# Performance work log

Measured on AMD Instinct MI355X. Metric: run time of the kernel, lower is better.

The kernel has to match this reference:

```python
import jax, jax.numpy as jnp
import numpy as np

N_NODES = 50000
N_EDGES = 800000
N_EVAL = 500000
D = 96


def _sage_conv(x, edge_index, W_l, W_r, b):
    # PyG SAGEConv with aggr='add':
    #   aggr_out[v] = sum_{(u->v) in edges} x[u]
    #   out = aggr_out @ W_l^T-equivalent + b + x @ W_r  (we store W as [in, out])
    src, dst = edge_index[0], edge_index[1]
    msgs = x[src]                                        # [E, d_in] irregular gather
    aggr = jax.ops.segment_sum(msgs, dst, num_segments=x.shape[0])  # [N, d_in]
    return aggr @ W_l + b + x @ W_r                      # [N, d_out]


def setup_inputs() -> dict:
    key = jax.random.key(0)
    ks = jax.random.split(key, 8)
    scale = 1.0 / np.sqrt(D)
    Features = jax.random.normal(ks[0], (N_NODES, D), dtype=jnp.float32)
    A = jax.random.randint(ks[1], (2, N_EDGES), 0, N_NODES, dtype=jnp.int64)
    E = jax.random.randint(ks[2], (2, N_EVAL), 0, N_NODES, dtype=jnp.int64)
    W1_l = jax.random.normal(ks[3], (D, D), dtype=jnp.float32) * scale
    W1_r = jax.random.normal(ks[4], (D, D), dtype=jnp.float32) * scale
    b1 = jnp.zeros((D,), dtype=jnp.float32)
    W2_l = jax.random.normal(ks[5], (D, D), dtype=jnp.float32) * scale
    W2_r = jax.random.normal(ks[6], (D, D), dtype=jnp.float32) * scale
    b2 = jnp.zeros((D,), dtype=jnp.float32)
    return {"Features": Features, "A": A, "E": E,
            "W1_l": W1_l, "W1_r": W1_r, "b1": b1,
            "W2_l": W2_l, "W2_r": W2_r, "b2": b2}


def reference(Features, A, E, W1_l, W1_r, b1, W2_l, W2_r, b2):
    h = _sage_conv(Features, A, W1_l, W1_r, b1)          # [N, hidden]
    h = jax.nn.relu(h)
    # dropout in eval mode = identity
    h = _sage_conv(h, A, W2_l, W2_r, b2)                 # [N, out]
    # edge scoring: gather src/dst embeddings, dot, sigmoid
    src = h[E[0]]                                        # [n_eval, out]
    dst = h[E[1]]                                        # [n_eval, out]
    return jax.nn.sigmoid(jnp.sum(src * dst, axis=-1))   # [n_eval]
```

## Files before the change

kernel.cpp:

```cpp
#include <hip/hip_runtime.h>
#include <math.h>

#define N_NODES 50000
#define N_EDGES 800000
#define N_EVAL  500000
#define CSTRIDE 16
#define MAXDEG  64
#define NB_GEMM ((N_NODES + 63) / 64)
#define NB_AGG  ((N_NODES * 24 + 255) / 256)
#define HALF_EVAL (N_EVAL / 2)

__device__ __forceinline__ float4 f4add(float4 a, float4 b) {
    return make_float4(a.x + b.x, a.y + b.y, a.z + b.z, a.w + b.w);
}
__device__ __forceinline__ float4 f4fma(float s, float4 w, float4 a) {
    return make_float4(fmaf(s, w.x, a.x), fmaf(s, w.y, a.y),
                       fmaf(s, w.z, a.z), fmaf(s, w.w, a.w));
}
__device__ __forceinline__ float4 ld4(const float* p) {
    return *(const float4*)p;
}


__device__ __forceinline__ void bucket_role(int idx, const int* __restrict__ src,
                                            const int* __restrict__ dst,
                                            int* __restrict__ degS,
                                            unsigned short* __restrict__ bucket) {
    int t = idx * 256 + threadIdx.x;
    if (t < N_EDGES / 4) {
        int4 s = ((const int4*)src)[t];
        int4 d = ((const int4*)dst)[t];
        int r0 = atomicAdd(&degS[(size_t)d.x * CSTRIDE], 1);
        int r1 = atomicAdd(&degS[(size_t)d.y * CSTRIDE], 1);
        int r2 = atomicAdd(&degS[(size_t)d.z * CSTRIDE], 1);
        int r3 = atomicAdd(&degS[(size_t)d.w * CSTRIDE], 1);
        if (r0 < MAXDEG) bucket[(size_t)d.x * MAXDEG + r0] = (unsigned short)s.x;
        if (r1 < MAXDEG) bucket[(size_t)d.y * MAXDEG + r1] = (unsigned short)s.y;
        if (r2 < MAXDEG) bucket[(size_t)d.z * MAXDEG + r2] = (unsigned short)s.z;
        if (r3 < MAXDEG) bucket[(size_t)d.w * MAXDEG + r3] = (unsigned short)s.w;
    }
}

__device__ __forceinline__ float4 aggr_compute16(int v, int c,
        const float* __restrict__ x, const int* __restrict__ degC,
        const unsigned short* __restrict__ bucket) {
    const float* xp = x + c * 4;
    const int4* bk4 = (const int4*)(bucket + (size_t)v * MAXDEG);
    int deg = degC[v];
    int4 p0 = bk4[0], p1 = bk4[1], p2 = bk4[2], p3 = bk4[3];
    int idx[32];
    idx[0]  = p0.x & 0xffff; idx[1]  = (int)((unsigned)p0.x >> 16);
    idx[2]  = p0.y & 0xffff; idx[3]  = (int)((unsigned)p0.y >> 16);
    idx[4]  = p0.z & 0xffff; idx[5]  = (int)((unsigned)p0.z >> 16);
    idx[6]  = p0.w & 0xffff; idx[7]  = (int)((unsigned)p0.w >> 16);
    idx[8]  = p1.x & 0xffff; idx[9]  = (int)((unsigned)p1.x >> 16);
    idx[10] = p1.y & 0xffff; idx[11] = (int)((unsigned)p1.y >> 16);
    idx[12] = p1.z & 0xffff; idx[13] = (int)((unsigned)p1.z >> 16);
    idx[14] = p1.w & 0xffff; idx[15] = (int)((unsigned)p1.w >> 16);
    idx[16] = p2.x & 0xffff; idx[17] = (int)((unsigned)p2.x >> 16);
    idx[18] = p2.y & 0xffff; idx[19] = (int)((unsigned)p2.y >> 16);
    idx[20] = p2.z & 0xffff; idx[21] = (int)((unsigned)p2.z >> 16);
    idx[22] = p2.w & 0xffff; idx[23] = (int)((unsigned)p2.w >> 16);
    idx[24] = p3.x & 0xffff; idx[25] = (int)((unsigned)p3.x >> 16);
    idx[26] = p3.y & 0xffff; idx[27] = (int)((unsigned)p3.y >> 16);
    idx[28] = p3.z & 0xffff; idx[29] = (int)((unsigned)p3.z >> 16);
    idx[30] = p3.w & 0xffff; idx[31] = (int)((unsigned)p3.w >> 16);

    const float4 z = make_float4(0.f, 0.f, 0.f, 0.f);
    float4 t0, t1, t2, t3, t4, t5, t6, t7, t8, t9, t10, t11, t12, t13, t14, t15;
    if (deg >= 16) {
        t0  = ld4(xp + (size_t)idx[0]  * 96);
        t1  = ld4(xp + (size_t)idx[1]  * 96);
        t2  = ld4(xp + (size_t)idx[2]  * 96);
        t3  = ld4(xp + (size_t)idx[3]  * 96);
        t4  = ld4(xp + (size_t)idx[4]  * 96);
        t5  = ld4(xp + (size_t)idx[5]  * 96);
        t6  = ld4(xp + (size_t)idx[6]  * 96);
        t7  = ld4(xp + (size_t)idx[7]  * 96);
        t8  = ld4(xp + (size_t)idx[8]  * 96);
        t9  = ld4(xp + (size_t)idx[9]  * 96);
        t10 = ld4(xp + (size_t)idx[10] * 96);
        t11 = ld4(xp + (size_t)idx[11] * 96);
        t12 = ld4(xp + (size_t)idx[12] * 96);
        t13 = ld4(xp + (size_t)idx[13] * 96);
        t14 = ld4(xp + (size_t)idx[14] * 96);
        t15 = ld4(xp + (size_t)idx[15] * 96);
    } else if (deg >= 8) {
        t0 = ld4(xp + (size_t)idx[0] * 96);
        t1 = ld4(xp + (size_t)idx[1] * 96);
        t2 = ld4(xp + (size_t)idx[2] * 96);
        t3 = ld4(xp + (size_t)idx[3] * 96);
        t4 = ld4(xp + (size_t)idx[4] * 96);
        t5 = ld4(xp + (size_t)idx[5] * 96);
        t6 = ld4(xp + (size_t)idx[6] * 96);
        t7 = ld4(xp + (size_t)idx[7] * 96);
        t8 = z; t9 = z; t10 = z; t11 = z; t12 = z; t13 = z; t14 = z; t15 = z;
        if (deg > 8)  t8  = ld4(xp + (size_t)idx[8]  * 96);
        if (deg > 9)  t9  = ld4(xp + (size_t)idx[9]  * 96);
        if (deg > 10) t10 = ld4(xp + (size_t)idx[10] * 96);
        if (deg > 11) t11 = ld4(xp + (size_t)idx[11] * 96);
        if (deg > 12) t12 = ld4(xp + (size_t)idx[12] * 96);
        if (deg > 13) t13 = ld4(xp + (size_t)idx[13] * 96);
        if (deg > 14) t14 = ld4(xp + (size_t)idx[14] * 96);
    } else {
        t0 = z; t1 = z; t2 = z; t3 = z; t4 = z; t5 = z; t6 = z; t7 = z;
        t8 = z; t9 = z; t10 = z; t11 = z; t12 = z; t13 = z; t14 = z; t15 = z;
        if (deg > 0) t0 = ld4(xp + (size_t)idx[0] * 96);
        if (deg > 1) t1 = ld4(xp + (size_t)idx[1] * 96);
        if (deg > 2) t2 = ld4(xp + (size_t)idx[2] * 96);
        if (deg > 3) t3 = ld4(xp + (size_t)idx[3] * 96);
        if (deg > 4) t4 = ld4(xp + (size_t)idx[4] * 96);
        if (deg > 5) t5 = ld4(xp + (size_t)idx[5] * 96);
        if (deg > 6) t6 = ld4(xp + (size_t)idx[6] * 96);
    }
    float4 a0 = f4add(f4add(f4add(t0, t1), f4add(t2, t3)),
                      f4add(f4add(t4, t5), f4add(t6, t7)));
    float4 a1 = f4add(f4add(f4add(t8, t9), f4add(t10, t11)),
                      f4add(f4add(t12, t13), f4add(t14, t15)));
    if (deg > 16) {
        float4 u0, u1, u2, u3, u4, u5, u6, u7;
        u0 = ld4(xp + (size_t)idx[16] * 96);
        u1 = z; u2 = z; u3 = z; u4 = z; u5 = z; u6 = z; u7 = z;
        if (deg > 17) u1 = ld4(xp + (size_t)idx[17] * 96);
        if (deg > 18) u2 = ld4(xp + (size_t)idx[18] * 96);
        if (deg > 19) u3 = ld4(xp + (size_t)idx[19] * 96);
        if (deg > 20) u4 = ld4(xp + (size_t)idx[20] * 96);
        if (deg > 21) u5 = ld4(xp + (size_t)idx[21] * 96);
        if (deg > 22) u6 = ld4(xp + (size_t)idx[22] * 96);
        if (deg > 23) u7 = ld4(xp + (size_t)idx[23] * 96);
        a0 = f4add(a0, f4add(f4add(u0, u1), f4add(u2, u3)));
        a1 = f4add(a1, f4add(f4add(u4, u5), f4add(u6, u7)));
    }
    if (deg > 24) {
        float4 u0, u1, u2, u3, u4, u5, u6, u7;
        u0 = ld4(xp + (size_t)idx[24] * 96);
        u1 = z; u2 = z; u3 = z; u4 = z; u5 = z; u6 = z; u7 = z;
        if (deg > 25) u1 = ld4(xp + (size_t)idx[25] * 96);
        if (deg > 26) u2 = ld4(xp + (size_t)idx[26] * 96);
        if (deg > 27) u3 = ld4(xp + (size_t)idx[27] * 96);
        if (deg > 28) u4 = ld4(xp + (size_t)idx[28] * 96);
        if (deg > 29) u5 = ld4(xp + (size_t)idx[29] * 96);
        if (deg > 30) u6 = ld4(xp + (size_t)idx[30] * 96);
        if (deg > 31) u7 = ld4(xp + (size_t)idx[31] * 96);
        a0 = f4add(a0, f4add(f4add(u0, u1), f4add(u2, u3)));
        a1 = f4add(a1, f4add(f4add(u4, u5), f4add(u6, u7)));
    }
    if (deg > 32) {
        const unsigned short* bk = bucket + (size_t)v * MAXDEG;
        for (int i = 32; i < deg; ++i)
            a0 = f4add(a0, ld4(xp + (size_t)bk[i] * 96));
    }
    return f4add(a0, a1);
}

__device__ __forceinline__ void aggr_role(int idx, const float* __restrict__ x,
                                          const int* __restrict__ degC,
                                          const unsigned short* __restrict__ bucket,
                                          float* __restrict__ out) {
    int gt = idx * 256 + threadIdx.x;
    if (gt >= N_NODES * 24) return;
    int v = gt / 24;
    int c = gt - v * 24;
    float4 res = aggr_compute16(v, c, x, degC, bucket);
    *(float4*)(out + (size_t)v * 96 + c * 4) = res;
}

__device__ __forceinline__ void selfgemm_role(int g, const float* __restrict__ X,
                                              const float* __restrict__ W96,
                                              const float* __restrict__ bias,
                                              float* __restrict__ S,
                                              float* __restrict__ Ws,
                                              float* __restrict__ xT) {
    const int tid = threadIdx.x;
    const int j   = tid & 31;
    const int ty  = tid >> 5;
    const int v0  = g * 64;

    float acc[8][3];
    float b0 = bias[j], b1 = bias[j + 32], b2 = bias[j + 64];
    #pragma unroll
    for (int r = 0; r < 8; ++r) { acc[r][0] = b0; acc[r][1] = b1; acc[r][2] = b2; }

    const int sr = tid >> 2;
    const int sc = tid & 3;
    int sv = v0 + sr; if (sv >= N_NODES) sv = N_NODES - 1;

    for (int kc = 0; kc < 3; ++kc) {
        const float* W = W96 + kc * (32 * 96);
        const int kbase = kc * 32;
        __syncthreads();
        #pragma unroll
        for (int i = 0; i < 3; ++i) {
            int f = tid + i * 256;
            *(float4*)(Ws + f * 4) = *(const float4*)(W + f * 4);
        }
        {
            const float* rowp = X + (size_t)sv * 96 + kbase;
            float4 a = *(const float4*)(rowp + sc * 4);
            float4 b = *(const float4*)(rowp + sc * 4 + 16);
            int k0 = sc * 4;
            xT[(k0 + 0) * 68 + sr] = a.x;
            xT[(k0 + 1) * 68 + sr] = a.y;
            xT[(k0 + 2) * 68 + sr] = a.z;
            xT[(k0 + 3) * 68 + sr] = a.w;
            xT[(k0 + 16) * 68 + sr] = b.x;
            xT[(k0 + 17) * 68 + sr] = b.y;
            xT[(k0 + 18) * 68 + sr] = b.z;
            xT[(k0 + 19) * 68 + sr] = b.w;
        }
        __syncthreads();
        #pragma unroll 8
        for (int kk = 0; kk < 32; ++kk) {
            float w0 = Ws[kk * 96 + j];
            float w1 = Ws[kk * 96 + j + 32];
            float w2 = Ws[kk * 96 + j + 64];
            float4 xa = *(const float4*)(xT + kk * 68 + ty * 8);
            float4 xb = *(const float4*)(xT + kk * 68 + ty * 8 + 4);
#define ROWFMA(r, xv)                                   \
            acc[r][0] = fmaf(xv, w0, acc[r][0]);        \
            acc[r][1] = fmaf(xv, w1, acc[r][1]);        \
            acc[r][2] = fmaf(xv, w2, acc[r][2]);
            ROWFMA(0, xa.x) ROWFMA(1, xa.y) ROWFMA(2, xa.z) ROWFMA(3, xa.w)
            ROWFMA(4, xb.x) ROWFMA(5, xb.y) ROWFMA(6, xb.z) ROWFMA(7, xb.w)
#undef ROWFMA
        }
    }
    #pragma unroll
    for (int r = 0; r < 8; ++r) {
        int v = v0 + ty * 8 + r;
        if (v < N_NODES) {
            S[(size_t)v * 96 + j]      = acc[r][0];
            S[(size_t)v * 96 + j + 32] = acc[r][1];
            S[(size_t)v * 96 + j + 64] = acc[r][2];
        }
    }
}


__global__ __launch_bounds__(256) void k_fusedA(const int* __restrict__ src,
                                                const int* __restrict__ dst,
                                                int* __restrict__ degS,
                                                unsigned short* __restrict__ bucket,
                                                const float* __restrict__ X,
                                                const float* __restrict__ Wr,
                                                const float* __restrict__ bias,
                                                float* __restrict__ S) {
    __shared__ float Ws[32 * 96];
    __shared__ float xT[32 * 68];
    int b = blockIdx.x;
    if (b & 1) selfgemm_role(b >> 1, X, Wr, bias, S, Ws, xT);
    else       bucket_role(b >> 1, src, dst, degS, bucket);
}

__global__ __launch_bounds__(256) void k_compact(const int* __restrict__ degS,
                                                 int* __restrict__ degC) {
    int v = blockIdx.x * 256 + threadIdx.x;
    if (v < N_NODES) {
        int d = degS[(size_t)v * CSTRIDE];
        degC[v] = d > MAXDEG ? MAXDEG : d;
    }
}

__global__ __launch_bounds__(256, 4) void k_aggr(const float* __restrict__ x,
                                                 const int* __restrict__ degC,
                                                 const unsigned short* __restrict__ bucket,
                                                 float* __restrict__ out) {
    aggr_role(blockIdx.x, x, degC, bucket, out);
}

__global__ __launch_bounds__(256, 4) void k_fusedC(const float* __restrict__ h1,
                                                   const int* __restrict__ degC,
                                                   const unsigned short* __restrict__ bucket,
                                                   float* __restrict__ aggrOut,
                                                   const float* __restrict__ Wr,
                                                   const float* __restrict__ bias,
                                                   float* __restrict__ S) {
    __shared__ float Ws[32 * 96];
    __shared__ float xT[32 * 68];
    int b = blockIdx.x;
    int g = b / 7, r = b % 7;
    if (r == 3) {
        if (g < NB_GEMM) selfgemm_role(g, h1, Wr, bias, S, Ws, xT);
    } else {
        int idx = g * 6 + (r < 3 ? r : r - 1);
        if (idx < NB_AGG) aggr_role(idx, h1, degC, bucket, aggrOut);
    }
}

template <int RELU>
__global__ __launch_bounds__(192) void k_gemmH(const float* __restrict__ P,
                                               const float* __restrict__ Wl,
                                               const float* __restrict__ S,
                                               float* __restrict__ out) {
    __shared__ float Ws[32 * 96];
    __shared__ float xT[32 * 68];
    const int tid = threadIdx.x;
    const int q   = tid % 24;
    const int rg  = tid / 24;
    const int v0  = blockIdx.x * 64;

    const int  row0 = tid >> 3,         qd0 = tid & 7;
    const int  row1 = (tid + 192) >> 3, qd1 = (tid + 192) & 7;
    const int  row2 = (tid + 384) >> 3, qd2 = (tid + 384) & 7;
    const bool has2 = (tid < 128);
    int sv0 = v0 + row0; if (sv0 >= N_NODES) sv0 = N_NODES - 1;
    int sv1 = v0 + row1; if (sv1 >= N_NODES) sv1 = N_NODES - 1;
    int sv2 = v0 + row2; if (sv2 >= N_NODES) sv2 = N_NODES - 1;

    float4 acc[8];
    #pragma unroll
    for (int r = 0; r < 8; ++r) acc[r] = make_float4(0.f, 0.f, 0.f, 0.f);

    float4 wreg0, wreg1, wreg2, wreg3;
    float4 xreg0, xreg1, xreg2;

    auto load_chunk = [&](int kc) {
        const float* W = Wl + kc * (32 * 96);
        const int kbase = kc * 32;
        wreg0 = *(const float4*)(W + (tid + 0 * 192) * 4);
        wreg1 = *(const float4*)(W + (tid + 1 * 192) * 4);
        wreg2 = *(const float4*)(W + (tid + 2 * 192) * 4);
        wreg3 = *(const float4*)(W + (tid + 3 * 192) * 4);
        xreg0 = *(const float4*)(P + (size_t)sv0 * 96 + kbase + qd0 * 4);
        xreg1 = *(const float4*)(P + (size_t)sv1 * 96 + kbase + qd1 * 4);
        if (has2) xreg2 = *(const float4*)(P + (size_t)sv2 * 96 + kbase + qd2 * 4);
    };
    auto store_chunk = [&]() {
        *(float4*)(Ws + (tid + 0 * 192) * 4) = wreg0;
        *(float4*)(Ws + (tid + 1 * 192) * 4) = wreg1;
        *(float4*)(Ws + (tid + 2 * 192) * 4) = wreg2;
        *(float4*)(Ws + (tid + 3 * 192) * 4) = wreg3;
        int k0 = qd0 * 4;
        xT[(k0 + 0) * 68 + row0] = xreg0.x;
        xT[(k0 + 1) * 68 + row0] = xreg0.y;
        xT[(k0 + 2) * 68 + row0] = xreg0.z;
        xT[(k0 + 3) * 68 + row0] = xreg0.w;
        int k1 = qd1 * 4;
        xT[(k1 + 0) * 68 + row1] = xreg1.x;
        xT[(k1 + 1) * 68 + row1] = xreg1.y;
        xT[(k1 + 2) * 68 + row1] = xreg1.z;
        xT[(k1 + 3) * 68 + row1] = xreg1.w;
        if (has2) {
            int k2 = qd2 * 4;
            xT[(k2 + 0) * 68 + row2] = xreg2.x;
            xT[(k2 + 1) * 68 + row2] = xreg2.y;
            xT[(k2 + 2) * 68 + row2] = xreg2.z;
            xT[(k2 + 3) * 68 + row2] = xreg2.w;
        }
    };

    load_chunk(0);
    for (int kc = 0; kc < 3; ++kc) {
        __syncthreads();
        store_chunk();
        if (kc < 2) load_chunk(kc + 1);
        __syncthreads();
        #pragma unroll 8
        for (int kk = 0; kk < 32; ++kk) {
            float4 w  = *(const float4*)(Ws + kk * 96 + q * 4);
            float4 xa = *(const float4*)(xT + kk * 68 + rg * 8);
            float4 xb = *(const float4*)(xT + kk * 68 + rg * 8 + 4);
            acc[0] = f4fma(xa.x, w, acc[0]);
            acc[1] = f4fma(xa.y, w, acc[1]);
            acc[2] = f4fma(xa.z, w, acc[2]);
            acc[3] = f4fma(xa.w, w, acc[3]);
            acc[4] = f4fma(xb.x, w, acc[4]);
            acc[5] = f4fma(xb.y, w, acc[5]);
            acc[6] = f4fma(xb.z, w, acc[6]);
            acc[7] = f4fma(xb.w, w, acc[7]);
        }
    }
    #pragma unroll
    for (int r = 0; r < 8; ++r) {
        int v = v0 + rg * 8 + r;
        if (v < N_NODES) {
            float4 s4 = *(const float4*)(S + (size_t)v * 96 + q * 4);
            float4 o = f4add(acc[r], s4);
            if (RELU) {
                o.x = fmaxf(o.x, 0.f); o.y = fmaxf(o.y, 0.f);
                o.z = fmaxf(o.z, 0.f); o.w = fmaxf(o.w, 0.f);
            }
            *(float4*)(out + (size_t)v * 96 + q * 4) = o;
        }
    }
}

__global__ __launch_bounds__(256) void k_score(const float* __restrict__ h,
                                               const int* __restrict__ E,
                                               float* __restrict__ out) {
    int t = blockIdx.x * 256 + threadIdx.x;
    int e = t >> 3, sub = t & 7;
    if (e >= HALF_EVAL) return;
    int e2 = e + HALF_EVAL;
    int s0 = E[e];
    int d0 = E[N_EVAL + e];
    int s1 = E[e2];
    int d1 = E[N_EVAL + e2];
    const float* ps0 = h + (size_t)s0 * 96 + sub * 12;
    const float* pd0 = h + (size_t)d0 * 96 + sub * 12;
    const float* ps1 = h + (size_t)s1 * 96 + sub * 12;
    const float* pd1 = h + (size_t)d1 * 96 + sub * 12;
    float4 a0 = ld4(ps0 + 0), a1 = ld4(ps0 + 4), a2 = ld4(ps0 + 8);
    float4 b0 = ld4(pd0 + 0), b1 = ld4(pd0 + 4), b2 = ld4(pd0 + 8);
    float4 c0 = ld4(ps1 + 0), c1 = ld4(ps1 + 4), c2 = ld4(ps1 + 8);
    float4 g0 = ld4(pd1 + 0), g1 = ld4(pd1 + 4), g2 = ld4(pd1 + 8);
    float dot0 = a0.x * b0.x + a0.y * b0.y + a0.z * b0.z + a0.w * b0.w
               + a1.x * b1.x + a1.y * b1.y + a1.z * b1.z + a1.w * b1.w
               + a2.x * b2.x + a2.y * b2.y + a2.z * b2.z + a2.w * b2.w;
    float dot1 = c0.x * g0.x + c0.y * g0.y + c0.z * g0.z + c0.w * g0.w
               + c1.x * g1.x + c1.y * g1.y + c1.z * g1.z + c1.w * g1.w
               + c2.x * g2.x + c2.y * g2.y + c2.z * g2.z + c2.w * g2.w;
    dot0 += __shfl_xor(dot0, 1, 64);
    dot1 += __shfl_xor(dot1, 1, 64);
    dot0 += __shfl_xor(dot0, 2, 64);
    dot1 += __shfl_xor(dot1, 2, 64);
    dot0 += __shfl_xor(dot0, 4, 64);
    dot1 += __shfl_xor(dot1, 4, 64);
    if (sub == 0) {
        out[e]  = 1.f / (1.f + expf(-dot0));
        out[e2] = 1.f / (1.f + expf(-dot1));
    }
}


extern "C" void kernel_launch(void* const* d_in, const int* in_sizes, int n_in,
                              void* d_out, int out_size, void* d_ws, size_t ws_size,
                              hipStream_t stream) {
    const float* Features = (const float*)d_in[0];
    const int*   A        = (const int*)d_in[1];
    const int*   E        = (const int*)d_in[2];
    const float* W1l = (const float*)d_in[3];
    const float* W1r = (const float*)d_in[4];
    const float* b1  = (const float*)d_in[5];
    const float* W2l = (const float*)d_in[6];
    const float* W2r = (const float*)d_in[7];
    const float* b2  = (const float*)d_in[8];
    float* out = (float*)d_out;

    char* p = (char*)d_ws;
    auto alloc = [&](size_t bytes) -> char* {
        char* q = p;
        p += (bytes + 255) & ~(size_t)255;
        return q;
    };
    int*   degS   = (int*)alloc((size_t)N_NODES * CSTRIDE * 4);
    int*   degC   = (int*)alloc((size_t)N_NODES * 4);
    unsigned short* bucket =
        (unsigned short*)alloc((size_t)N_NODES * MAXDEG * 2);
    float* bufA   = (float*)alloc((size_t)N_NODES * 96 * 4);
    float* bufB   = (float*)alloc((size_t)N_NODES * 96 * 4);
    float* bufS   = (float*)alloc((size_t)N_NODES * 96 * 4);

    const int* Asrc = A;
    const int* Adst = A + N_EDGES;

    hipMemsetAsync(degS, 0, (size_t)N_NODES * CSTRIDE * 4, stream);

    k_fusedA<<<2 * NB_GEMM, 256, 0, stream>>>(Asrc, Adst, degS, bucket,
                                              Features, W1r, b1, bufS);
    k_compact<<<(N_NODES + 255) / 256, 256, 0, stream>>>(degS, degC);
    k_aggr<<<NB_AGG, 256, 0, stream>>>(Features, degC, bucket, bufA);
    k_gemmH<1><<<NB_GEMM, 192, 0, stream>>>(bufA, W1l, bufS, bufB);
    k_fusedC<<<7 * NB_GEMM, 256, 0, stream>>>(bufB, degC, bucket, bufA,
                                              W2r, b2, bufS);
    k_gemmH<0><<<NB_GEMM, 192, 0, stream>>>(bufA, W2l, bufS, bufA);
    k_score<<<(HALF_EVAL * 8 + 255) / 256, 256, 0, stream>>>(bufA, E, out);
}
```

Before: 300.2 us.

## Drop compaction kernel, shrink GEMM k-chunks, raise occupancy, use nontemporal stores

Removes the k_compact launch and makes the aggregation read the strided degree array directly, clamping the degree inline. The self-GEMM now uses 16-wide k chunks, which halves its shared-memory footprint, and launch bounds rise to 8 blocks per SM for the fused and aggregation kernels. Output stores switch to nontemporal stores. The risks are higher register pressure under the tighter launch bounds, more syncs per GEMM, strided degree reads that are less coalesced, and nontemporal stores evicting data that later kernels reread.

```diff
diff --git a/kernel.cpp b/kernel.cpp
--- a/kernel.cpp
+++ b/kernel.cpp
@@ -19,6 +19,12 @@
 }
 __device__ __forceinline__ float4 ld4(const float* p) {
     return *(const float4*)p;
+}
+typedef float fnt4 __attribute__((ext_vector_type(4)));
+__device__ __forceinline__ void st4nt(float* p, float4 v) {
+    fnt4 t;
+    t.x = v.x; t.y = v.y; t.z = v.z; t.w = v.w;
+    __builtin_nontemporal_store(t, (fnt4*)p);
 }
 
 
@@ -42,12 +48,13 @@
 }
 
 __device__ __forceinline__ float4 aggr_compute16(int v, int c,
-        const float* __restrict__ x, const int* __restrict__ degC,
+        const float* __restrict__ x, const int* __restrict__ degS,
         const unsigned short* __restrict__ bucket) {
     const float* xp = x + c * 4;
     const int4* bk4 = (const int4*)(bucket + (size_t)v * MAXDEG);
-    int deg = degC[v];
+    int deg = degS[(size_t)v * CSTRIDE];
     int4 p0 = bk4[0], p1 = bk4[1], p2 = bk4[2], p3 = bk4[3];
+    if (deg > MAXDEG) deg = MAXDEG;
     int idx[32];
     idx[0]  = p0.x & 0xffff; idx[1]  = (int)((unsigned)p0.x >> 16);
     idx[2]  = p0.y & 0xffff; idx[3]  = (int)((unsigned)p0.y >> 16);
@@ -154,15 +161,15 @@
 }
 
 __device__ __forceinline__ void aggr_role(int idx, const float* __restrict__ x,
-                                          const int* __restrict__ degC,
+                                          const int* __restrict__ degS,
                                           const unsigned short* __restrict__ bucket,
                                           float* __restrict__ out) {
     int gt = idx * 256 + threadIdx.x;
     if (gt >= N_NODES * 24) return;
     int v = gt / 24;
     int c = gt - v * 24;
-    float4 res = aggr_compute16(v, c, x, degC, bucket);
-    *(float4*)(out + (size_t)v * 96 + c * 4) = res;
+    float4 res = aggr_compute16(v, c, x, degS, bucket);
+    st4nt(out + (size_t)v * 96 + c * 4, res);
 }
 
 __device__ __forceinline__ void selfgemm_role(int g, const float* __restrict__ X,
@@ -185,32 +192,24 @@
     const int sc = tid & 3;
     int sv = v0 + sr; if (sv >= N_NODES) sv = N_NODES - 1;
 
-    for (int kc = 0; kc < 3; ++kc) {
-        const float* W = W96 + kc * (32 * 96);
-        const int kbase = kc * 32;
+    for (int kc = 0; kc < 6; ++kc) {
+        const float* W = W96 + kc * (16 * 96);
+        const int kbase = kc * 16;
         __syncthreads();
-        #pragma unroll
-        for (int i = 0; i < 3; ++i) {
-            int f = tid + i * 256;
-            *(float4*)(Ws + f * 4) = *(const float4*)(W + f * 4);
-        }
+        *(float4*)(Ws + tid * 4) = ld4(W + tid * 4);
+        if (tid < 128)
+            *(float4*)(Ws + (tid + 256) * 4) = ld4(W + (tid + 256) * 4);
         {
-            const float* rowp = X + (size_t)sv * 96 + kbase;
-            float4 a = *(const float4*)(rowp + sc * 4);
-            float4 b = *(const float4*)(rowp + sc * 4 + 16);
+            float4 a = ld4(X + (size_t)sv * 96 + kbase + sc * 4);
             int k0 = sc * 4;
             xT[(k0 + 0) * 68 + sr] = a.x;
             xT[(k0 + 1) * 68 + sr] = a.y;
             xT[(k0 + 2) * 68 + sr] = a.z;
             xT[(k0 + 3) * 68 + sr] = a.w;
-            xT[(k0 + 16) * 68 + sr] = b.x;
-            xT[(k0 + 17) * 68 + sr] = b.y;
-            xT[(k0 + 18) * 68 + sr] = b.z;
-            xT[(k0 + 19) * 68 + sr] = b.w;
         }
         __syncthreads();
         #pragma unroll 8
-        for (int kk = 0; kk < 32; ++kk) {
+        for (int kk = 0; kk < 16; ++kk) {
             float w0 = Ws[kk * 96 + j];
             float w1 = Ws[kk * 96 + j + 32];
             float w2 = Ws[kk * 96 + j + 64];
@@ -229,61 +228,52 @@
     for (int r = 0; r < 8; ++r) {
         int v = v0 + ty * 8 + r;
         if (v < N_NODES) {
-            S[(size_t)v * 96 + j]      = acc[r][0];
-            S[(size_t)v * 96 + j + 32] = acc[r][1];
-            S[(size_t)v * 96 + j + 64] = acc[r][2];
-        }
-    }
-}
-
-
-__global__ __launch_bounds__(256) void k_fusedA(const int* __restrict__ src,
-                                                const int* __restrict__ dst,
-                                                int* __restrict__ degS,
-                                                unsigned short* __restrict__ bucket,
-                                                const float* __restrict__ X,
-                                                const float* __restrict__ Wr,
-                                                const float* __restrict__ bias,
-                                                float* __restrict__ S) {
-    __shared__ float Ws[32 * 96];
-    __shared__ float xT[32 * 68];
+            __builtin_nontemporal_store(acc[r][0], &S[(size_t)v * 96 + j]);
+            __builtin_nontemporal_store(acc[r][1], &S[(size_t)v * 96 + j + 32]);
+            __builtin_nontemporal_store(acc[r][2], &S[(size_t)v * 96 + j + 64]);
+        }
+    }
+}
+
+
+__global__ __launch_bounds__(256, 8) void k_fusedA(const int* __restrict__ src,
+                                                   const int* __restrict__ dst,
+                                                   int* __restrict__ degS,
+                                                   unsigned short* __restrict__ bucket,
+                                                   const float* __restrict__ X,
+                                                   const float* __restrict__ Wr,
+                                                   const float* __restrict__ bias,
+                                                   float* __restrict__ S) {
+    __shared__ float Ws[16 * 96];
+    __shared__ float xT[16 * 68];
     int b = blockIdx.x;
     if (b & 1) selfgemm_role(b >> 1, X, Wr, bias, S, Ws, xT);
     else       bucket_role(b >> 1, src, dst, degS, bucket);
 }
 
-__global__ __launch_bounds__(256) void k_compact(const int* __restrict__ degS,
-                                                 int* __restrict__ degC) {
-    int v = blockIdx.x * 256 + threadIdx.x;
-    if (v < N_NODES) {
-        int d = degS[(size_t)v * CSTRIDE];
-        degC[v] = d > MAXDEG ? MAXDEG : d;
-    }
-}
-
-__global__ __launch_bounds__(256, 4) void k_aggr(const float* __restrict__ x,
-                                                 const int* __restrict__ degC,
+__global__ __launch_bounds__(256, 8) void k_aggr(const float* __restrict__ x,
+                                                 const int* __restrict__ degS,
                                                  const unsigned short* __restrict__ bucket,
                                                  float* __restrict__ out) {
-    aggr_role(blockIdx.x, x, degC, bucket, out);
-}
-
-__global__ __launch_bounds__(256, 4) void k_fusedC(const float* __restrict__ h1,
-                                                   const int* __restrict__ degC,
+    aggr_role(blockIdx.x, x, degS, bucket, out);
+}
+
+__global__ __launch_bounds__(256, 8) void k_fusedC(const float* __restrict__ h1,
+                                                   const int* __restrict__ degS,
                                                    const unsigned short* __restrict__ bucket,
                                                    float* __restrict__ aggrOut,
                                                    const float* __restrict__ Wr,
                                                    const float* __restrict__ bias,
                                                    float* __restrict__ S) {
-    __shared__ float Ws[32 * 96];
-    __shared__ float xT[32 * 68];
+    __shared__ float Ws[16 * 96];
+    __shared__ float xT[16 * 68];
     int b = blockIdx.x;
     int g = b / 7, r = b % 7;
     if (r == 3) {
         if (g < NB_GEMM) selfgemm_role(g, h1, Wr, bias, S, Ws, xT);
     } else {
         int idx = g * 6 + (r < 3 ? r : r - 1);
-        if (idx < NB_AGG) aggr_role(idx, h1, degC, bucket, aggrOut);
+        if (idx < NB_AGG) aggr_role(idx, h1, degS, bucket, aggrOut);
     }
 }
 
@@ -380,7 +370,7 @@
                 o.x = fmaxf(o.x, 0.f); o.y = fmaxf(o.y, 0.f);
                 o.z = fmaxf(o.z, 0.f); o.w = fmaxf(o.w, 0.f);
             }
-            *(float4*)(out + (size_t)v * 96 + q * 4) = o;
+            st4nt(out + (size_t)v * 96 + q * 4, o);
         }
     }
 }
@@ -444,7 +434,6 @@
         return q;
     };
     int*   degS   = (int*)alloc((size_t)N_NODES * CSTRIDE * 4);
-    int*   degC   = (int*)alloc((size_t)N_NODES * 4);
     unsigned short* bucket =
         (unsigned short*)alloc((size_t)N_NODES * MAXDEG * 2);
     float* bufA   = (float*)alloc((size_t)N_NODES * 96 * 4);
@@ -458,10 +447,9 @@
 
     k_fusedA<<<2 * NB_GEMM, 256, 0, stream>>>(Asrc, Adst, degS, bucket,
                                               Features, W1r, b1, bufS);
-    k_compact<<<(N_NODES + 255) / 256, 256, 0, stream>>>(degS, degC);
-    k_aggr<<<NB_AGG, 256, 0, stream>>>(Features, degC, bucket, bufA);
+    k_aggr<<<NB_AGG, 256, 0, stream>>>(Features, degS, bucket, bufA);
     k_gemmH<1><<<NB_GEMM, 192, 0, stream>>>(bufA, W1l, bufS, bufB);
-    k_fusedC<<<7 * NB_GEMM, 256, 0, stream>>>(bufB, degC, bucket, bufA,
+    k_fusedC<<<7 * NB_GEMM, 256, 0, stream>>>(bufB, degS, bucket, bufA,
                                               W2r, b2, bufS);
     k_gemmH<0><<<NB_GEMM, 192, 0, stream>>>(bufA, W2l, bufS, bufA);
     k_score<<<(HALF_EVAL * 8 + 255) / 256, 256, 0, stream>>>(bufA, E, out);
```

Result: slower. 409.9 us (+36.5%).
